# Kernel tuning notes

Hardware: AMD Instinct MI355X
Metric: run time of the kernel (lower is better)

Reference implementation:

```python
import jax, jax.numpy as jnp
import numpy as np

TAU = 0.5
EPS = 1e-12  # F.normalize default eps


def _projection(z, fc1_w, fc1_b, fc2_w, fc2_b):
    h = jax.nn.elu(z @ fc1_w.T + fc1_b)
    return h @ fc2_w.T + fc2_b


def _normalize(z):
    n = jnp.linalg.norm(z, axis=1, keepdims=True)
    return z / jnp.maximum(n, EPS)


def _semi_loss(h1, h2):
    z1 = _normalize(h1)
    z2 = _normalize(h2)
    refl_sim = jnp.exp((z1 @ z1.T) / TAU)      # [N, N]
    between_sim = jnp.exp((z1 @ z2.T) / TAU)   # [N, N]
    pos = jnp.diagonal(between_sim)
    denom = refl_sim.sum(axis=1) + between_sim.sum(axis=1) - jnp.diagonal(refl_sim)
    return -jnp.log(pos / denom)


def setup_inputs() -> dict:
    key = jax.random.key(0)
    k1, k2, k3, k4 = jax.random.split(key, 4)
    N, H, P = 8192, 512, 512
    s1 = 1.0 / np.sqrt(H)
    s2 = 1.0 / np.sqrt(P)
    return {
        "z1": jax.random.normal(k1, (N, H), jnp.float32),
        "z2": jax.random.normal(k2, (N, H), jnp.float32),
        "fc1_w": jax.random.normal(k3, (P, H), jnp.float32) * s1,
        "fc1_b": jnp.zeros((P,), jnp.float32),
        "fc2_w": jax.random.normal(k4, (H, P), jnp.float32) * s2,
        "fc2_b": jnp.zeros((H,), jnp.float32),
    }


def reference(z1, z2, fc1_w, fc1_b, fc2_w, fc2_b):
    h1 = _projection(z1, fc1_w, fc1_b, fc2_w, fc2_b)
    h2 = _projection(z2, fc1_w, fc1_b, fc2_w, fc2_b)
    l1 = _semi_loss(h1, h2)
    l2 = _semi_loss(h2, h1)
    ret = (l1 + l2) * 0.5
    return ret.mean()
```

## Files before the change

### kernel.cpp

```cpp
#include <hip/hip_runtime.h>
#include <math.h>

typedef __attribute__((ext_vector_type(8))) __bf16 bf16x8;
typedef __attribute__((ext_vector_type(4))) float f32x4;
typedef __attribute__((ext_vector_type(16))) float f32x16;
typedef __attribute__((ext_vector_type(8))) unsigned short u16x8;
typedef __attribute__((ext_vector_type(8))) int i32x8;

#define GAS(p) ((const __attribute__((address_space(1))) void*)(p))
#define LAS(p) ((__attribute__((address_space(3))) void*)(p))

__device__ __forceinline__ unsigned short f2bf(float f) {
  union { float f; unsigned int u; } v; v.f = f;
  unsigned int r = (v.u + 0x7FFFu + ((v.u >> 16) & 1u)) >> 16;
  return (unsigned short)r;
}
__device__ __forceinline__ float bf2f(unsigned short b) {
  union { unsigned int u; float f; } v; v.u = ((unsigned int)b) << 16;
  return v.f;
}

__global__ __launch_bounds__(256) void cast_all_kernel(
    const float* __restrict__ z1, const float* __restrict__ z2,
    const float* __restrict__ w1, const float* __restrict__ w2,
    unsigned short* __restrict__ z1b, unsigned short* __restrict__ z2b,
    unsigned short* __restrict__ w1b, unsigned short* __restrict__ w2b) {
  int b = blockIdx.x;
  const float* in; unsigned short* out; int base;
  if (b < 4096)       { in = z1; out = z1b; base = b; }
  else if (b < 8192)  { in = z2; out = z2b; base = b - 4096; }
  else if (b < 8448)  { in = w1; out = w1b; base = b - 8192; }
  else                { in = w2; out = w2b; base = b - 8448; }
  int i = (base * 256 + threadIdx.x) * 4;
  float4 v = *(const float4*)(in + i);
  ushort4 o;
  o.x = f2bf(v.x); o.y = f2bf(v.y); o.z = f2bf(v.z); o.w = f2bf(v.w);
  *(ushort4*)(out + i) = o;
}

__device__ __forceinline__ void gemm_tile_512(
    const unsigned short* __restrict__ A, const unsigned short* __restrict__ B,
    int m0, int n0, unsigned short* lA, unsigned short* lB, f32x4 acc[4][4]) {
  constexpr int K = 512;
  const int tid  = threadIdx.x;
  const int wave = tid >> 6;
  const int lane = tid & 63;
  const int quad = lane >> 4;
  const int l16  = lane & 15;
  const int wrow = (wave & 1) * 64;
  const int wcol = (wave >> 1) * 64;

  const f32x4 zero = {0.f, 0.f, 0.f, 0.f};
#pragma unroll
  for (int i = 0; i < 4; ++i)
#pragma unroll
    for (int j = 0; j < 4; ++j) acc[i][j] = zero;

  const int e0 = wave * 1024 + lane * 8;
  const int r0 = e0 >> 5, c0 = e0 & 31;
  const int e1 = e0 + 512;
  const int r1 = e1 >> 5, c1 = e1 & 31;

  const unsigned short* Ag0 = A + (size_t)(m0 + r0) * K + c0;
  const unsigned short* Ag1 = A + (size_t)(m0 + r1) * K + c1;
  const unsigned short* Bg0 = B + (size_t)(n0 + r0) * K + c0;
  const unsigned short* Bg1 = B + (size_t)(n0 + r1) * K + c1;

  for (int kt = 0; kt < K; kt += 32) {
    __syncthreads();
    __builtin_amdgcn_global_load_lds(GAS(Ag0 + kt), LAS(&lA[e0]), 16, 0, 0);
    __builtin_amdgcn_global_load_lds(GAS(Ag1 + kt), LAS(&lA[e1]), 16, 0, 0);
    __builtin_amdgcn_global_load_lds(GAS(Bg0 + kt), LAS(&lB[e0]), 16, 0, 0);
    __builtin_amdgcn_global_load_lds(GAS(Bg1 + kt), LAS(&lB[e1]), 16, 0, 0);
    __syncthreads();

    bf16x8 af[4], bfr[4];
#pragma unroll
    for (int i = 0; i < 4; ++i) {
      af[i]  = *(const bf16x8*)&lA[(wrow + i * 16 + l16) * 32 + quad * 8];
      bfr[i] = *(const bf16x8*)&lB[(wcol + i * 16 + l16) * 32 + quad * 8];
    }
#pragma unroll
    for (int mi = 0; mi < 4; ++mi)
#pragma unroll
      for (int ni = 0; ni < 4; ++ni)
        acc[mi][ni] = __builtin_amdgcn_mfma_f32_16x16x32_bf16(
            af[mi], bfr[ni], acc[mi][ni], 0, 0, 0);
  }
}

template<int EPI>
__global__ __launch_bounds__(256)
void proj_kernel(const unsigned short* __restrict__ A1,
                 const unsigned short* __restrict__ A2,
                 const unsigned short* __restrict__ W,
                 const float* __restrict__ bias,
                 unsigned short* __restrict__ C1,
                 unsigned short* __restrict__ C2) {
  __shared__ unsigned short lA[128 * 32];
  __shared__ unsigned short lB[128 * 32];
  const int b = blockIdx.x;
  const int which = b >> 8;
  const int r = b & 255;
  const int n0 = (r & 3) * 128;
  const int m0 = (r >> 2) * 128;
  const unsigned short* A = which ? A2 : A1;
  unsigned short* C = which ? C2 : C1;

  f32x4 acc[4][4];
  gemm_tile_512(A, W, m0, n0, lA, lB, acc);

  const int lane = threadIdx.x & 63;
  const int wave = threadIdx.x >> 6;
  const int quad = lane >> 4;
  const int l16  = lane & 15;
  const int wrow = (wave & 1) * 64;
  const int wcol = (wave >> 1) * 64;

#pragma unroll
  for (int ni = 0; ni < 4; ++ni) {
    const int c = n0 + wcol + ni * 16 + l16;
    const float bv = bias[c];
#pragma unroll
    for (int mi = 0; mi < 4; ++mi) {
      const int rbase = m0 + wrow + mi * 16 + quad * 4;
#pragma unroll
      for (int rr = 0; rr < 4; ++rr) {
        float v = acc[mi][ni][rr] + bv;
        if constexpr (EPI == 0) v = (v > 0.f) ? v : expm1f(v);
        C[(size_t)(rbase + rr) * 512 + c] = f2bf(v);
      }
    }
  }
}

__global__ __launch_bounds__(256, 2)
void gram_kernel(const unsigned char* __restrict__ q1,
                 const unsigned char* __restrict__ q2,
                 float* __restrict__ d11, float* __restrict__ d22,
                 float* __restrict__ d12r, float* __restrict__ d12c) {
  __shared__ unsigned char lA[65536];
  __shared__ unsigned char lB[16384];

  const int b = blockIdx.x;
  const unsigned char *Abase, *Bbase;
  float *rptr, *cptr;
  int by, g, cnt;
  bool cross;
  if (b < 1088) {
    const bool first = (b < 544);
    int j = first ? b : b - 544;
    int q = (int)((sqrtf(2.f * j + 1.f) - 1.f) * 0.5f);
    while (2 * (q + 1) * (q + 2) <= j) ++q;
    while (2 * q * (q + 1) > j) --q;
    const int w = j - 2 * q * (q + 1);
    const int dr = w / (q + 1);
    g = w - dr * (q + 1);
    by = 4 * q + dr;
    const unsigned char* h = first ? q1 : q2;
    Abase = h; Bbase = h;
    rptr = first ? d11 : d22; cptr = rptr;
    cnt = min(4, by + 1 - g * 4);
    cross = false;
  } else {
    const int j = b - 1088;
    g = j >> 6; by = j & 63;
    Abase = q1; Bbase = q2;
    rptr = d12r; cptr = d12c;
    cnt = 4; cross = true;
  }

  const int tid  = threadIdx.x;
  const int wave = tid >> 6;
  const int lane = tid & 63;
  const int half = lane >> 5;
  const int l31  = lane & 31;
  const int pa0 = (wave & 1) * 2;
  const int pb0 = (wave >> 1) * 2;
  const int lfo = half * 1024 + l31 * 16;

  const unsigned char* Asrc = Abase + (size_t)(by * 4 + wave) * 16384 + lane * 16;
  unsigned char* Adst = lA + wave * 16384 + lane * 16;
  unsigned char* Bdst = lB + wave * 4096 + lane * 16;

  union frag { i32x8 v; int4 h[2]; };

  float rs[2][16];
#pragma unroll
  for (int mi = 0; mi < 2; ++mi)
#pragma unroll
    for (int rr = 0; rr < 16; ++rr) rs[mi][rr] = 0.f;

  for (int t = 0; t < cnt; ++t) {
    const int ct = g * 4 + t;
    const unsigned char* Bsrc = Bbase + (size_t)(ct * 4 + wave) * 16384 + lane * 16;

    f32x16 acc[2][2];
#pragma unroll
    for (int i = 0; i < 2; ++i)
#pragma unroll
      for (int jj = 0; jj < 2; ++jj)
#pragma unroll
        for (int rr = 0; rr < 16; ++rr) acc[i][jj][rr] = 0.f;

    for (int KT = 0; KT < 4; ++KT) {
      __syncthreads();
      if (t == 0) {
#pragma unroll
        for (int i = 0; i < 4; ++i)
          __builtin_amdgcn_global_load_lds(GAS(Asrc + KT * 4096 + i * 1024),
                                           LAS(Adst + KT * 4096 + i * 1024), 16, 0, 0);
      }
#pragma unroll
      for (int i = 0; i < 4; ++i)
        __builtin_amdgcn_global_load_lds(GAS(Bsrc + KT * 4096 + i * 1024),
                                         LAS(Bdst + i * 1024), 16, 0, 0);
      __syncthreads();

#pragma unroll
      for (int ktl = 0; ktl < 2; ++ktl) {
        frag fa[2], fb[2];
#pragma unroll
        for (int i = 0; i < 2; ++i) {
          const int oa = (pa0 + i) * 16384 + KT * 4096 + ktl * 2048 + lfo;
          const int ob = (pb0 + i) * 4096 + ktl * 2048 + lfo;
          fa[i].h[0] = *(const int4*)&lA[oa];
          fa[i].h[1] = *(const int4*)&lA[oa + 512];
          fb[i].h[0] = *(const int4*)&lB[ob];
          fb[i].h[1] = *(const int4*)&lB[ob + 512];
        }
#pragma unroll
        for (int mi = 0; mi < 2; ++mi)
#pragma unroll
          for (int ni = 0; ni < 2; ++ni)
            acc[mi][ni] = __builtin_amdgcn_mfma_scale_f32_32x32x64_f8f6f4(
                fa[mi].v, fb[ni].v, acc[mi][ni],
                0, 0,
                0, 0x7F7F7F7F,
                0, 0x7F7F7F7F);
      }
    }

    float cs[2] = {0.f, 0.f};
#pragma unroll
    for (int mi = 0; mi < 2; ++mi)
#pragma unroll
      for (int ni = 0; ni < 2; ++ni)
#pragma unroll
        for (int rr = 0; rr < 16; ++rr) {
          float v = __expf(2.0f * acc[mi][ni][rr]);
          rs[mi][rr] += v;
          cs[ni] += v;
        }
    const bool diag = (!cross) && (ct == by);
    if (!diag) {
#pragma unroll
      for (int ni = 0; ni < 2; ++ni) {
        float v = cs[ni] + __shfl_xor(cs[ni], 32, 64);
        if (half == 0)
          atomicAdd(&cptr[ct * 128 + (wave >> 1) * 64 + ni * 32 + l31], v);
      }
    }
  }

#pragma unroll
  for (int mi = 0; mi < 2; ++mi) {
#pragma unroll
    for (int d = 1; d < 32; d <<= 1) {
#pragma unroll
      for (int rr = 0; rr < 16; ++rr) rs[mi][rr] += __shfl_xor(rs[mi][rr], d, 64);
    }
    if (l31 == 0) {
      const int mb = by * 128 + (wave & 1) * 64 + mi * 32;
#pragma unroll
      for (int rr = 0; rr < 16; ++rr) {
        const int row = mb + (rr & 3) + 8 * (rr >> 2) + 4 * half;
        atomicAdd(&rptr[row], rs[mi][rr]);
      }
    }
  }
}

__global__ __launch_bounds__(256)
void norm_diag_kernel(const unsigned short* __restrict__ h1,
                      const unsigned short* __restrict__ h2,
                      unsigned char* __restrict__ q1,
                      unsigned char* __restrict__ q2,
                      float* __restrict__ cdiag) {
  const int wave = threadIdx.x >> 6, lane = threadIdx.x & 63;
  const int row = blockIdx.x * 4 + wave;
  const u16x8 u1 = *(const u16x8*)(h1 + (size_t)row * 512 + lane * 8);
  const u16x8 u2 = *(const u16x8*)(h2 + (size_t)row * 512 + lane * 8);
  float f1[8], f2[8], ss1 = 0.f, ss2 = 0.f;
#pragma unroll
  for (int j = 0; j < 8; ++j) {
    f1[j] = bf2f(u1[j]); ss1 += f1[j] * f1[j];
    f2[j] = bf2f(u2[j]); ss2 += f2[j] * f2[j];
  }
#pragma unroll
  for (int d = 1; d < 64; d <<= 1) {
    ss1 += __shfl_xor(ss1, d, 64);
    ss2 += __shfl_xor(ss2, d, 64);
  }
  const float inv1 = 1.0f / fmaxf(sqrtf(ss1), 1e-12f);
  const float inv2 = 1.0f / fmaxf(sqrtf(ss2), 1e-12f);
  float a[8], bb[8];
  float dot = 0.f;
#pragma unroll
  for (int j = 0; j < 8; ++j) {
    a[j] = f1[j] * inv1; bb[j] = f2[j] * inv2;
    dot += a[j] * bb[j];
  }
  int lo1 = __builtin_amdgcn_cvt_pk_fp8_f32(a[0], a[1], 0, false);
  lo1 = __builtin_amdgcn_cvt_pk_fp8_f32(a[2], a[3], lo1, true);
  int hi1 = __builtin_amdgcn_cvt_pk_fp8_f32(a[4], a[5], 0, false);
  hi1 = __builtin_amdgcn_cvt_pk_fp8_f32(a[6], a[7], hi1, true);
  int lo2 = __builtin_amdgcn_cvt_pk_fp8_f32(bb[0], bb[1], 0, false);
  lo2 = __builtin_amdgcn_cvt_pk_fp8_f32(bb[2], bb[3], lo2, true);
  int hi2 = __builtin_amdgcn_cvt_pk_fp8_f32(bb[4], bb[5], 0, false);
  hi2 = __builtin_amdgcn_cvt_pk_fp8_f32(bb[6], bb[7], hi2, true);

  const int c0 = lane * 8;
  const size_t dst = (size_t)(row >> 5) * 16384 + (c0 >> 6) * 2048
                   + ((c0 >> 4) & 3) * 512 + (row & 31) * 16 + (c0 & 15);
  *(int2*)(q1 + dst) = make_int2(lo1, hi1);
  *(int2*)(q2 + dst) = make_int2(lo2, hi2);
#pragma unroll
  for (int d = 1; d < 64; d <<= 1) dot += __shfl_xor(dot, d, 64);
  if (lane == 0) cdiag[row] = dot;
}

__global__ __launch_bounds__(256)
void finalize_kernel(const float* __restrict__ d11, const float* __restrict__ d22,
                     const float* __restrict__ d12r, const float* __restrict__ d12c,
                     const float* __restrict__ cdiag, float* __restrict__ out) {
  const float e2 = 7.38905609893065f;
  float s = 0.f;
  for (int i = threadIdx.x; i < 8192; i += 256) {
    const float den1 = d11[i] + d12r[i] - e2;
    const float den2 = d22[i] + d12c[i] - e2;
    s += -2.0f * cdiag[i] + 0.5f * (logf(den1) + logf(den2));
  }
#pragma unroll
  for (int d = 1; d < 64; d <<= 1) s += __shfl_xor(s, d, 64);
  __shared__ float sm[4];
  if ((threadIdx.x & 63) == 0) sm[threadIdx.x >> 6] = s;
  __syncthreads();
  if (threadIdx.x == 0) out[0] = (sm[0] + sm[1] + sm[2] + sm[3]) * (1.0f / 8192.0f);
}

extern "C" void kernel_launch(void* const* d_in, const int* in_sizes, int n_in,
                              void* d_out, int out_size, void* d_ws, size_t ws_size,
                              hipStream_t stream) {
  const float* z1 = (const float*)d_in[0];
  const float* z2 = (const float*)d_in[1];
  const float* w1 = (const float*)d_in[2];
  const float* b1 = (const float*)d_in[3];
  const float* w2 = (const float*)d_in[4];
  const float* b2 = (const float*)d_in[5];
  float* out = (float*)d_out;

  const int N = 8192, D = 512;
  char* ws = (char*)d_ws;
  auto alloc = [&](size_t bytes) {
    char* p = ws; ws += (bytes + 255) & ~(size_t)255; return p;
  };
  unsigned short* z1b = (unsigned short*)alloc((size_t)N * D * 2);
  unsigned short* z2b = (unsigned short*)alloc((size_t)N * D * 2);
  unsigned short* g1  = (unsigned short*)alloc((size_t)N * D * 2);
  unsigned short* g2  = (unsigned short*)alloc((size_t)N * D * 2);
  unsigned short* w1b = (unsigned short*)alloc((size_t)D * D * 2);
  unsigned short* w2b = (unsigned short*)alloc((size_t)D * D * 2);
  float* sums  = (float*)alloc((size_t)4 * N * sizeof(float));
  float* cdiag = (float*)alloc((size_t)N * sizeof(float));
  float* d11 = sums, *d22 = sums + N, *d12r = sums + 2 * N, *d12c = sums + 3 * N;
  unsigned short* h1 = z1b;
  unsigned short* h2 = z2b;
  unsigned char* q1 = (unsigned char*)g1;
  unsigned char* q2 = (unsigned char*)g2;

  hipMemsetAsync(sums, 0, (size_t)4 * N * sizeof(float), stream);

  cast_all_kernel<<<dim3(8704), 256, 0, stream>>>(z1, z2, w1, w2, z1b, z2b, w1b, w2b);
  proj_kernel<0><<<dim3(512), 256, 0, stream>>>(z1b, z2b, w1b, b1, g1, g2);
  proj_kernel<1><<<dim3(512), 256, 0, stream>>>(g1, g2, w2b, b2, h1, h2);
  norm_diag_kernel<<<dim3(N / 4), 256, 0, stream>>>(h1, h2, q1, q2, cdiag);
  gram_kernel<<<dim3(2112), 256, 0, stream>>>(q1, q2, d11, d22, d12r, d12c);
  finalize_kernel<<<1, 256, 0, stream>>>(d11, d22, d12r, d12c, cdiag, out);
}
```

Baseline: 240.6 us.

## Enlarge gram tile to 256 rows with double-buffered B and XCD-aware scheduling

The gram kernel now runs 512-thread blocks that each own a 256-row A panel, held in 128KB of dynamic LDS, against 128-column B tiles. B loads are double-buffered, so the next K slice is prefetched while MFMAs run, which removes one barrier per step. Blocks are remapped so jobs spread across XCDs and triangular work is balanced by pairing jobs from both ends. This halves the block count and raises reuse of the A fragments, at the cost of 160KB of LDS per block, which limits occupancy to one block per CU, and some wasted compute on the diagonal tiles in the triangular case.

```diff
diff --git a/kernel.cpp b/kernel.cpp
--- a/kernel.cpp
+++ b/kernel.cpp
@@ -134,149 +134,169 @@
   }
 }
 
-__global__ __launch_bounds__(256, 2)
+__global__ __launch_bounds__(512, 2)
 void gram_kernel(const unsigned char* __restrict__ q1,
                  const unsigned char* __restrict__ q2,
                  float* __restrict__ d11, float* __restrict__ d22,
                  float* __restrict__ d12r, float* __restrict__ d12c) {
-  __shared__ unsigned char lA[65536];
-  __shared__ unsigned char lB[16384];
+  extern __shared__ unsigned char lds[];
+  unsigned char* lA = lds;
+  unsigned char* lB = lds + 131072;
 
   const int b = blockIdx.x;
   const unsigned char *Abase, *Bbase;
   float *rptr, *cptr;
-  int by, g, cnt;
+  int R, g, cnt;
   bool cross;
-  if (b < 1088) {
-    const bool first = (b < 544);
-    int j = first ? b : b - 544;
-    int q = (int)((sqrtf(2.f * j + 1.f) - 1.f) * 0.5f);
-    while (2 * (q + 1) * (q + 2) <= j) ++q;
-    while (2 * q * (q + 1) > j) --q;
-    const int w = j - 2 * q * (q + 1);
-    const int dr = w / (q + 1);
-    g = w - dr * (q + 1);
-    by = 4 * q + dr;
-    const unsigned char* h = first ? q1 : q2;
+  if (b < 544) {
+    const int xcd = b & 7, loc = b >> 3;
+    const int job = xcd * 68 + loc;
+    const bool v2 = (job >= 272);
+    const int j = v2 ? (543 - job) : job;
+    int p = 0;
+    while (p < 31) {
+      const int pn = p + 1, m = pn >> 1;
+      const int Cn = (pn & 1) ? (m + 1) * (m + 1) : m * (m + 1);
+      if (Cn <= j) ++p; else break;
+    }
+    const int m = p >> 1;
+    const int Cp = (p & 1) ? (m + 1) * (m + 1) : m * (m + 1);
+    g = j - Cp;
+    R = p * 256;
+    cnt = min(4, (2 * p + 2) - 4 * g);
+    const unsigned char* h = v2 ? q2 : q1;
     Abase = h; Bbase = h;
-    rptr = first ? d11 : d22; cptr = rptr;
-    cnt = min(4, by + 1 - g * 4);
+    rptr = v2 ? d22 : d11; cptr = rptr;
     cross = false;
   } else {
-    const int j = b - 1088;
-    g = j >> 6; by = j & 63;
+    const int i = b - 544;
+    const int xcd = i & 7, loc = i >> 3;
+    g = 2 * xcd + (loc >> 5);
+    R = (loc & 31) * 256;
+    cnt = 4;
     Abase = q1; Bbase = q2;
     rptr = d12r; cptr = d12c;
-    cnt = 4; cross = true;
-  }
-
-  const int tid  = threadIdx.x;
-  const int wave = tid >> 6;
-  const int lane = tid & 63;
+    cross = true;
+  }
+
+  const int wave = threadIdx.x >> 6;
+  const int lane = threadIdx.x & 63;
   const int half = lane >> 5;
   const int l31  = lane & 31;
-  const int pa0 = (wave & 1) * 2;
-  const int pb0 = (wave >> 1) * 2;
-  const int lfo = half * 1024 + l31 * 16;
-
-  const unsigned char* Asrc = Abase + (size_t)(by * 4 + wave) * 16384 + lane * 16;
+  const int rt_w = (R >> 7) + (wave >> 2);
+  const int lfo  = half * 1024 + l31 * 16;
+
+  const unsigned char* Asrc = Abase + (size_t)((R >> 5) + wave) * 16384 + lane * 16;
   unsigned char* Adst = lA + wave * 16384 + lane * 16;
-  unsigned char* Bdst = lB + wave * 4096 + lane * 16;
+  const int bseg = (wave >> 1) * 4096 + (wave & 1) * 2048 + lane * 16;
 
   union frag { i32x8 v; int4 h[2]; };
 
-  float rs[2][16];
-#pragma unroll
-  for (int mi = 0; mi < 2; ++mi)
-#pragma unroll
-    for (int rr = 0; rr < 16; ++rr) rs[mi][rr] = 0.f;
+  float rs[16];
+#pragma unroll
+  for (int rr = 0; rr < 16; ++rr) rs[rr] = 0.f;
+
+  {
+    const unsigned char* Bs = Bbase + (size_t)(g * 16 + (wave >> 1)) * 16384
+                            + (wave & 1) * 2048 + lane * 16;
+    __builtin_amdgcn_global_load_lds(GAS(Bs), LAS(lB + bseg), 16, 0, 0);
+    __builtin_amdgcn_global_load_lds(GAS(Bs + 1024), LAS(lB + bseg + 1024), 16, 0, 0);
+#pragma unroll
+    for (int i = 0; i < 4; ++i)
+      __builtin_amdgcn_global_load_lds(GAS(Asrc + i * 1024),
+                                       LAS(Adst + i * 1024), 16, 0, 0);
+  }
+  __syncthreads();
 
   for (int t = 0; t < cnt; ++t) {
     const int ct = g * 4 + t;
-    const unsigned char* Bsrc = Bbase + (size_t)(ct * 4 + wave) * 16384 + lane * 16;
-
-    f32x16 acc[2][2];
-#pragma unroll
-    for (int i = 0; i < 2; ++i)
-#pragma unroll
-      for (int jj = 0; jj < 2; ++jj)
-#pragma unroll
-        for (int rr = 0; rr < 16; ++rr) acc[i][jj][rr] = 0.f;
-
+
+    f32x16 acc[4];
+#pragma unroll
+    for (int ni = 0; ni < 4; ++ni)
+#pragma unroll
+      for (int rr = 0; rr < 16; ++rr) acc[ni][rr] = 0.f;
+
+#pragma unroll
     for (int KT = 0; KT < 4; ++KT) {
+      if (KT < 3) {
+        const unsigned char* Bs = Bbase + (size_t)(ct * 4 + (wave >> 1)) * 16384
+                                + (KT + 1) * 4096 + (wave & 1) * 2048 + lane * 16;
+        unsigned char* bd = lB + ((KT + 1) & 1) * 16384 + bseg;
+        __builtin_amdgcn_global_load_lds(GAS(Bs), LAS(bd), 16, 0, 0);
+        __builtin_amdgcn_global_load_lds(GAS(Bs + 1024), LAS(bd + 1024), 16, 0, 0);
+        if (t == 0) {
+#pragma unroll
+          for (int i = 0; i < 4; ++i)
+            __builtin_amdgcn_global_load_lds(
+                GAS(Asrc + (KT + 1) * 4096 + i * 1024),
+                LAS(Adst + (KT + 1) * 4096 + i * 1024), 16, 0, 0);
+        }
+      } else if (t + 1 < cnt) {
+        const unsigned char* Bs = Bbase + (size_t)((ct + 1) * 4 + (wave >> 1)) * 16384
+                                + (wave & 1) * 2048 + lane * 16;
+        unsigned char* bd = lB + bseg;
+        __builtin_amdgcn_global_load_lds(GAS(Bs), LAS(bd), 16, 0, 0);
+        __builtin_amdgcn_global_load_lds(GAS(Bs + 1024), LAS(bd + 1024), 16, 0, 0);
+      }
+
+      const unsigned char* bufB = lB + (KT & 1) * 16384;
+#pragma unroll
+      for (int ktl = 0; ktl < 2; ++ktl) {
+        frag fa, fb[4];
+        const int oa = wave * 16384 + KT * 4096 + ktl * 2048 + lfo;
+        fa.h[0] = *(const int4*)&lA[oa];
+        fa.h[1] = *(const int4*)&lA[oa + 512];
+#pragma unroll
+        for (int ni = 0; ni < 4; ++ni) {
+          const int ob = ni * 4096 + ktl * 2048 + lfo;
+          fb[ni].h[0] = *(const int4*)&bufB[ob];
+          fb[ni].h[1] = *(const int4*)&bufB[ob + 512];
+        }
+#pragma unroll
+        for (int ni = 0; ni < 4; ++ni)
+          acc[ni] = __builtin_amdgcn_mfma_scale_f32_32x32x64_f8f6f4(
+              fa.v, fb[ni].v, acc[ni],
+              0, 0,
+              0, 0x7F7F7F7F,
+              0, 0x7F7F7F7F);
+      }
       __syncthreads();
-      if (t == 0) {
-#pragma unroll
-        for (int i = 0; i < 4; ++i)
-          __builtin_amdgcn_global_load_lds(GAS(Asrc + KT * 4096 + i * 1024),
-                                           LAS(Adst + KT * 4096 + i * 1024), 16, 0, 0);
-      }
-#pragma unroll
-      for (int i = 0; i < 4; ++i)
-        __builtin_amdgcn_global_load_lds(GAS(Bsrc + KT * 4096 + i * 1024),
-                                         LAS(Bdst + i * 1024), 16, 0, 0);
-      __syncthreads();
-
-#pragma unroll
-      for (int ktl = 0; ktl < 2; ++ktl) {
-        frag fa[2], fb[2];
-#pragma unroll
-        for (int i = 0; i < 2; ++i) {
-          const int oa = (pa0 + i) * 16384 + KT * 4096 + ktl * 2048 + lfo;
-          const int ob = (pb0 + i) * 4096 + ktl * 2048 + lfo;
-          fa[i].h[0] = *(const int4*)&lA[oa];
-          fa[i].h[1] = *(const int4*)&lA[oa + 512];
-          fb[i].h[0] = *(const int4*)&lB[ob];
-          fb[i].h[1] = *(const int4*)&lB[ob + 512];
-        }
-#pragma unroll
-        for (int mi = 0; mi < 2; ++mi)
-#pragma unroll
-          for (int ni = 0; ni < 2; ++ni)
-            acc[mi][ni] = __builtin_amdgcn_mfma_scale_f32_32x32x64_f8f6f4(
-                fa[mi].v, fb[ni].v, acc[mi][ni],
-                0, 0,
-                0, 0x7F7F7F7F,
-                0, 0x7F7F7F7F);
-      }
-    }
-
-    float cs[2] = {0.f, 0.f};
-#pragma unroll
-    for (int mi = 0; mi < 2; ++mi)
-#pragma unroll
-      for (int ni = 0; ni < 2; ++ni)
+    }
+
+    const bool valid = cross || (ct <= rt_w);
+    const bool docol = cross || (ct < rt_w);
+    if (valid) {
+      float cs[4] = {0.f, 0.f, 0.f, 0.f};
+#pragma unroll
+      for (int ni = 0; ni < 4; ++ni)
 #pragma unroll
         for (int rr = 0; rr < 16; ++rr) {
-          float v = __expf(2.0f * acc[mi][ni][rr]);
-          rs[mi][rr] += v;
+          const float v = __expf(2.0f * acc[ni][rr]);
+          rs[rr] += v;
           cs[ni] += v;
         }
-    const bool diag = (!cross) && (ct == by);
-    if (!diag) {
-#pragma unroll
-      for (int ni = 0; ni < 2; ++ni) {
-        float v = cs[ni] + __shfl_xor(cs[ni], 32, 64);
-        if (half == 0)
-          atomicAdd(&cptr[ct * 128 + (wave >> 1) * 64 + ni * 32 + l31], v);
+      if (docol) {
+#pragma unroll
+        for (int ni = 0; ni < 4; ++ni) {
+          const float v = cs[ni] + __shfl_xor(cs[ni], 32, 64);
+          if (half == 0) atomicAdd(&cptr[ct * 128 + ni * 32 + l31], v);
+        }
       }
     }
   }
 
 #pragma unroll
-  for (int mi = 0; mi < 2; ++mi) {
-#pragma unroll
-    for (int d = 1; d < 32; d <<= 1) {
-#pragma unroll
-      for (int rr = 0; rr < 16; ++rr) rs[mi][rr] += __shfl_xor(rs[mi][rr], d, 64);
-    }
-    if (l31 == 0) {
-      const int mb = by * 128 + (wave & 1) * 64 + mi * 32;
-#pragma unroll
-      for (int rr = 0; rr < 16; ++rr) {
-        const int row = mb + (rr & 3) + 8 * (rr >> 2) + 4 * half;
-        atomicAdd(&rptr[row], rs[mi][rr]);
-      }
+  for (int d = 1; d < 32; d <<= 1) {
+#pragma unroll
+    for (int rr = 0; rr < 16; ++rr) rs[rr] += __shfl_xor(rs[rr], d, 64);
+  }
+  if (l31 == 0) {
+    const int rb = R + wave * 32;
+#pragma unroll
+    for (int rr = 0; rr < 16; ++rr) {
+      const int row = rb + (rr & 3) + 8 * (rr >> 2) + 4 * half;
+      atomicAdd(&rptr[row], rs[rr]);
     }
   }
 }
@@ -381,10 +401,13 @@
 
   hipMemsetAsync(sums, 0, (size_t)4 * N * sizeof(float), stream);
 
+  hipFuncSetAttribute((const void*)gram_kernel,
+                      hipFuncAttributeMaxDynamicSharedMemorySize, 163840);
+
   cast_all_kernel<<<dim3(8704), 256, 0, stream>>>(z1, z2, w1, w2, z1b, z2b, w1b, w2b);
   proj_kernel<0><<<dim3(512), 256, 0, stream>>>(z1b, z2b, w1b, b1, g1, g2);
   proj_kernel<1><<<dim3(512), 256, 0, stream>>>(g1, g2, w2b, b2, h1, h2);
   norm_diag_kernel<<<dim3(N / 4), 256, 0, stream>>>(h1, h2, q1, q2, cdiag);
-  gram_kernel<<<dim3(2112), 256, 0, stream>>>(q1, q2, d11, d22, d12r, d12c);
+  gram_kernel<<<dim3(1056), 512, 163840, stream>>>(q1, q2, d11, d22, d12r, d12c);
   finalize_kernel<<<1, 256, 0, stream>>>(d11, d22, d12r, d12c, cdiag, out);
 }
```

New measurement: 563.5 us. 134% more time.

## Fuse input fp32 cast into first projection GEMM and double-buffer gram B loads

Applied to the files above, without the earlier changes.

The separate cast of z1/z2 to bf16 is removed. The first projection GEMM now loads fp32 activations directly and converts them to bf16 while writing LDS, which saves a full read and write pass over the inputs. Separately, the FP8 gram kernel moves to a finer K step with double-buffered B tiles in LDS and prefetches the next step during the MFMA work, so each step needs one barrier instead of two. The fp32 path uses register-staged loads instead of direct global-to-LDS loads, which may raise latency inside the projection kernel.

```diff
diff --git a/kernel.cpp b/kernel.cpp
--- a/kernel.cpp
+++ b/kernel.cpp
@@ -20,17 +20,13 @@
   return v.f;
 }
 
-__global__ __launch_bounds__(256) void cast_all_kernel(
-    const float* __restrict__ z1, const float* __restrict__ z2,
+__global__ __launch_bounds__(256) void cast_w_kernel(
     const float* __restrict__ w1, const float* __restrict__ w2,
-    unsigned short* __restrict__ z1b, unsigned short* __restrict__ z2b,
     unsigned short* __restrict__ w1b, unsigned short* __restrict__ w2b) {
   int b = blockIdx.x;
   const float* in; unsigned short* out; int base;
-  if (b < 4096)       { in = z1; out = z1b; base = b; }
-  else if (b < 8192)  { in = z2; out = z2b; base = b - 4096; }
-  else if (b < 8448)  { in = w1; out = w1b; base = b - 8192; }
-  else                { in = w2; out = w2b; base = b - 8448; }
+  if (b < 256) { in = w1; out = w1b; base = b; }
+  else         { in = w2; out = w2b; base = b - 256; }
   int i = (base * 256 + threadIdx.x) * 4;
   float4 v = *(const float4*)(in + i);
   ushort4 o;
@@ -38,8 +34,9 @@
   *(ushort4*)(out + i) = o;
 }
 
-__device__ __forceinline__ void gemm_tile_512(
-    const unsigned short* __restrict__ A, const unsigned short* __restrict__ B,
+template<bool AF32>
+__device__ __forceinline__ void gemm_tile_512x(
+    const void* __restrict__ Av, const unsigned short* __restrict__ B,
     int m0, int n0, unsigned short* lA, unsigned short* lB, f32x4 acc[4][4]) {
   constexpr int K = 512;
   const int tid  = threadIdx.x;
@@ -61,15 +58,33 @@
   const int e1 = e0 + 512;
   const int r1 = e1 >> 5, c1 = e1 & 31;
 
-  const unsigned short* Ag0 = A + (size_t)(m0 + r0) * K + c0;
-  const unsigned short* Ag1 = A + (size_t)(m0 + r1) * K + c1;
+  const unsigned short* Ab = (const unsigned short*)Av;
+  const float*          Af = (const float*)Av;
+  const unsigned short* Ag0 = Ab + (size_t)(m0 + r0) * K + c0;
+  const unsigned short* Ag1 = Ab + (size_t)(m0 + r1) * K + c1;
+  const float*          Af0 = Af + (size_t)(m0 + r0) * K + c0;
+  const float*          Af1 = Af + (size_t)(m0 + r1) * K + c1;
   const unsigned short* Bg0 = B + (size_t)(n0 + r0) * K + c0;
   const unsigned short* Bg1 = B + (size_t)(n0 + r1) * K + c1;
 
   for (int kt = 0; kt < K; kt += 32) {
     __syncthreads();
-    __builtin_amdgcn_global_load_lds(GAS(Ag0 + kt), LAS(&lA[e0]), 16, 0, 0);
-    __builtin_amdgcn_global_load_lds(GAS(Ag1 + kt), LAS(&lA[e1]), 16, 0, 0);
+    if constexpr (AF32) {
+      const float4 a0 = *(const float4*)(Af0 + kt);
+      const float4 a1 = *(const float4*)(Af0 + kt + 4);
+      const float4 b0 = *(const float4*)(Af1 + kt);
+      const float4 b1 = *(const float4*)(Af1 + kt + 4);
+      u16x8 p0, p1;
+      p0[0]=f2bf(a0.x); p0[1]=f2bf(a0.y); p0[2]=f2bf(a0.z); p0[3]=f2bf(a0.w);
+      p0[4]=f2bf(a1.x); p0[5]=f2bf(a1.y); p0[6]=f2bf(a1.z); p0[7]=f2bf(a1.w);
+      p1[0]=f2bf(b0.x); p1[1]=f2bf(b0.y); p1[2]=f2bf(b0.z); p1[3]=f2bf(b0.w);
+      p1[4]=f2bf(b1.x); p1[5]=f2bf(b1.y); p1[6]=f2bf(b1.z); p1[7]=f2bf(b1.w);
+      *(u16x8*)&lA[e0] = p0;
+      *(u16x8*)&lA[e1] = p1;
+    } else {
+      __builtin_amdgcn_global_load_lds(GAS(Ag0 + kt), LAS(&lA[e0]), 16, 0, 0);
+      __builtin_amdgcn_global_load_lds(GAS(Ag1 + kt), LAS(&lA[e1]), 16, 0, 0);
+    }
     __builtin_amdgcn_global_load_lds(GAS(Bg0 + kt), LAS(&lB[e0]), 16, 0, 0);
     __builtin_amdgcn_global_load_lds(GAS(Bg1 + kt), LAS(&lB[e1]), 16, 0, 0);
     __syncthreads();
@@ -91,8 +106,8 @@
 
 template<int EPI>
 __global__ __launch_bounds__(256)
-void proj_kernel(const unsigned short* __restrict__ A1,
-                 const unsigned short* __restrict__ A2,
+void proj_kernel(const void* __restrict__ A1,
+                 const void* __restrict__ A2,
                  const unsigned short* __restrict__ W,
                  const float* __restrict__ bias,
                  unsigned short* __restrict__ C1,
@@ -104,11 +119,11 @@
   const int r = b & 255;
   const int n0 = (r & 3) * 128;
   const int m0 = (r >> 2) * 128;
-  const unsigned short* A = which ? A2 : A1;
+  const void* A = which ? A2 : A1;
   unsigned short* C = which ? C2 : C1;
 
   f32x4 acc[4][4];
-  gemm_tile_512(A, W, m0, n0, lA, lB, acc);
+  gemm_tile_512x<EPI == 0>(A, W, m0, n0, lA, lB, acc);
 
   const int lane = threadIdx.x & 63;
   const int wave = threadIdx.x >> 6;
@@ -140,7 +155,7 @@
                  float* __restrict__ d11, float* __restrict__ d22,
                  float* __restrict__ d12r, float* __restrict__ d12c) {
   __shared__ unsigned char lA[65536];
-  __shared__ unsigned char lB[16384];
+  __shared__ unsigned char lB[2][8192];
 
   const int b = blockIdx.x;
   const unsigned char *Abase, *Bbase;
@@ -181,7 +196,6 @@
 
   const unsigned char* Asrc = Abase + (size_t)(by * 4 + wave) * 16384 + lane * 16;
   unsigned char* Adst = lA + wave * 16384 + lane * 16;
-  unsigned char* Bdst = lB + wave * 4096 + lane * 16;
 
   union frag { i32x8 v; int4 h[2]; };
 
@@ -190,10 +204,19 @@
   for (int mi = 0; mi < 2; ++mi)
 #pragma unroll
     for (int rr = 0; rr < 16; ++rr) rs[mi][rr] = 0.f;
+
+  {
+    __builtin_amdgcn_global_load_lds(GAS(Asrc), LAS(Adst), 16, 0, 0);
+    __builtin_amdgcn_global_load_lds(GAS(Asrc + 1024), LAS(Adst + 1024), 16, 0, 0);
+    const unsigned char* Bs = Bbase + (size_t)(g * 4 * 4 + wave) * 16384 + lane * 16;
+    unsigned char* bd = lB[0] + wave * 2048 + lane * 16;
+    __builtin_amdgcn_global_load_lds(GAS(Bs), LAS(bd), 16, 0, 0);
+    __builtin_amdgcn_global_load_lds(GAS(Bs + 1024), LAS(bd + 1024), 16, 0, 0);
+  }
+  __syncthreads();
 
   for (int t = 0; t < cnt; ++t) {
     const int ct = g * 4 + t;
-    const unsigned char* Bsrc = Bbase + (size_t)(ct * 4 + wave) * 16384 + lane * 16;
 
     f32x16 acc[2][2];
 #pragma unroll
@@ -203,42 +226,49 @@
 #pragma unroll
         for (int rr = 0; rr < 16; ++rr) acc[i][jj][rr] = 0.f;
 
-    for (int KT = 0; KT < 4; ++KT) {
+#pragma unroll
+    for (int KT = 0; KT < 8; ++KT) {
+      if (t == 0 && KT < 7) {
+        __builtin_amdgcn_global_load_lds(GAS(Asrc + (KT + 1) * 2048),
+                                         LAS(Adst + (KT + 1) * 2048), 16, 0, 0);
+        __builtin_amdgcn_global_load_lds(GAS(Asrc + (KT + 1) * 2048 + 1024),
+                                         LAS(Adst + (KT + 1) * 2048 + 1024), 16, 0, 0);
+      }
+      if (KT < 7) {
+        const unsigned char* Bs = Bbase + (size_t)(ct * 4 + wave) * 16384
+                                + (KT + 1) * 2048 + lane * 16;
+        unsigned char* bd = lB[(KT + 1) & 1] + wave * 2048 + lane * 16;
+        __builtin_amdgcn_global_load_lds(GAS(Bs), LAS(bd), 16, 0, 0);
+        __builtin_amdgcn_global_load_lds(GAS(Bs + 1024), LAS(bd + 1024), 16, 0, 0);
+      } else if (t + 1 < cnt) {
+        const unsigned char* Bs = Bbase + (size_t)((ct + 1) * 4 + wave) * 16384
+                                + lane * 16;
+        unsigned char* bd = lB[0] + wave * 2048 + lane * 16;
+        __builtin_amdgcn_global_load_lds(GAS(Bs), LAS(bd), 16, 0, 0);
+        __builtin_amdgcn_global_load_lds(GAS(Bs + 1024), LAS(bd + 1024), 16, 0, 0);
+      }
+
+      const unsigned char* bufB = lB[KT & 1];
+      frag fa[2], fb[2];
+#pragma unroll
+      for (int i = 0; i < 2; ++i) {
+        const int oa = (pa0 + i) * 16384 + KT * 2048 + lfo;
+        const int ob = (pb0 + i) * 2048 + lfo;
+        fa[i].h[0] = *(const int4*)&lA[oa];
+        fa[i].h[1] = *(const int4*)&lA[oa + 512];
+        fb[i].h[0] = *(const int4*)&bufB[ob];
+        fb[i].h[1] = *(const int4*)&bufB[ob + 512];
+      }
+#pragma unroll
+      for (int mi = 0; mi < 2; ++mi)
+#pragma unroll
+        for (int ni = 0; ni < 2; ++ni)
+          acc[mi][ni] = __builtin_amdgcn_mfma_scale_f32_32x32x64_f8f6f4(
+              fa[mi].v, fb[ni].v, acc[mi][ni],
+              0, 0,
+              0, 0x7F7F7F7F,
+              0, 0x7F7F7F7F);
       __syncthreads();
-      if (t == 0) {
-#pragma unroll
-        for (int i = 0; i < 4; ++i)
-          __builtin_amdgcn_global_load_lds(GAS(Asrc + KT * 4096 + i * 1024),
-                                           LAS(Adst + KT * 4096 + i * 1024), 16, 0, 0);
-      }
-#pragma unroll
-      for (int i = 0; i < 4; ++i)
-        __builtin_amdgcn_global_load_lds(GAS(Bsrc + KT * 4096 + i * 1024),
-                                         LAS(Bdst + i * 1024), 16, 0, 0);
-      __syncthreads();
-
-#pragma unroll
-      for (int ktl = 0; ktl < 2; ++ktl) {
-        frag fa[2], fb[2];
-#pragma unroll
-        for (int i = 0; i < 2; ++i) {
-          const int oa = (pa0 + i) * 16384 + KT * 4096 + ktl * 2048 + lfo;
-          const int ob = (pb0 + i) * 4096 + ktl * 2048 + lfo;
-          fa[i].h[0] = *(const int4*)&lA[oa];
-          fa[i].h[1] = *(const int4*)&lA[oa + 512];
-          fb[i].h[0] = *(const int4*)&lB[ob];
-          fb[i].h[1] = *(const int4*)&lB[ob + 512];
-        }
-#pragma unroll
-        for (int mi = 0; mi < 2; ++mi)
-#pragma unroll
-          for (int ni = 0; ni < 2; ++ni)
-            acc[mi][ni] = __builtin_amdgcn_mfma_scale_f32_32x32x64_f8f6f4(
-                fa[mi].v, fb[ni].v, acc[mi][ni],
-                0, 0,
-                0, 0x7F7F7F7F,
-                0, 0x7F7F7F7F);
-      }
     }
 
     float cs[2] = {0.f, 0.f};
@@ -365,8 +395,8 @@
   auto alloc = [&](size_t bytes) {
     char* p = ws; ws += (bytes + 255) & ~(size_t)255; return p;
   };
-  unsigned short* z1b = (unsigned short*)alloc((size_t)N * D * 2);
-  unsigned short* z2b = (unsigned short*)alloc((size_t)N * D * 2);
+  unsigned short* h1  = (unsigned short*)alloc((size_t)N * D * 2);
+  unsigned short* h2  = (unsigned short*)alloc((size_t)N * D * 2);
   unsigned short* g1  = (unsigned short*)alloc((size_t)N * D * 2);
   unsigned short* g2  = (unsigned short*)alloc((size_t)N * D * 2);
   unsigned short* w1b = (unsigned short*)alloc((size_t)D * D * 2);
@@ -374,16 +404,16 @@
   float* sums  = (float*)alloc((size_t)4 * N * sizeof(float));
   float* cdiag = (float*)alloc((size_t)N * sizeof(float));
   float* d11 = sums, *d22 = sums + N, *d12r = sums + 2 * N, *d12c = sums + 3 * N;
-  unsigned short* h1 = z1b;
-  unsigned short* h2 = z2b;
   unsigned char* q1 = (unsigned char*)g1;
   unsigned char* q2 = (unsigned char*)g2;
 
   hipMemsetAsync(sums, 0, (size_t)4 * N * sizeof(float), stream);
 
-  cast_all_kernel<<<dim3(8704), 256, 0, stream>>>(z1, z2, w1, w2, z1b, z2b, w1b, w2b);
-  proj_kernel<0><<<dim3(512), 256, 0, stream>>>(z1b, z2b, w1b, b1, g1, g2);
-  proj_kernel<1><<<dim3(512), 256, 0, stream>>>(g1, g2, w2b, b2, h1, h2);
+  cast_w_kernel<<<dim3(512), 256, 0, stream>>>(w1, w2, w1b, w2b);
+  proj_kernel<0><<<dim3(512), 256, 0, stream>>>((const void*)z1, (const void*)z2,
+                                                w1b, b1, g1, g2);
+  proj_kernel<1><<<dim3(512), 256, 0, stream>>>((const void*)g1, (const void*)g2,
+                                                w2b, b2, h1, h2);
   norm_diag_kernel<<<dim3(N / 4), 256, 0, stream>>>(h1, h2, q1, q2, cdiag);
   gram_kernel<<<dim3(2112), 256, 0, stream>>>(q1, q2, d11, d22, d12r, d12c);
   finalize_kernel<<<1, 256, 0, stream>>>(d11, d22, d12r, d12c, cdiag, out);
```

Result: slower. 313.8 us (+30.4%).
